# Kernel optimization log

Measured on AMD Instinct MI355X. Metric: run time of the kernel, lower is better.

The kernel has to match this reference:

```python
import jax, jax.numpy as jnp
import numpy as np

B, N, D_IN, D_OUT, E = 2, 50000, 128, 64, 800000
NEG_SLOPE = 0.2  # LeakyReLU negative slope (alpha)


def setup_inputs() -> dict:
    key = jax.random.key(0)
    ks = jax.random.split(key, 8)
    X_key = jax.random.normal(ks[0], (B, N, D_IN), dtype=jnp.float32)
    X_value = jax.random.normal(ks[1], (B, N, D_IN), dtype=jnp.float32)
    src = jax.random.randint(ks[2], (E,), 0, N, dtype=jnp.int32)
    dst = jnp.sort(jax.random.randint(ks[3], (E,), 0, N, dtype=jnp.int32))
    s = 1.0 / np.sqrt(D_IN)
    Wk = jax.random.normal(ks[4], (D_IN, D_OUT), dtype=jnp.float32) * s
    bk = jnp.zeros((D_OUT,), dtype=jnp.float32)
    Wv = jax.random.normal(ks[5], (D_IN, D_OUT), dtype=jnp.float32) * s
    bv = jnp.zeros((D_OUT,), dtype=jnp.float32)
    return {"X_key": X_key, "X_value": X_value, "Wk": Wk, "bk": bk,
            "Wv": Wv, "bv": bv, "src": src, "dst": dst}


def reference(X_key, X_value, Wk, bk, Wv, bv, src, dst):
    n = X_key.shape[1]
    h_key = X_key @ Wk + bk      # [B, N, D_OUT]
    h_value = X_value @ Wv + bv  # [B, N, D_OUT]

    def per_batch(hk, hv):
        # per-edge dot-product attention score
        e = jnp.sum(hk[src] * hk[dst], axis=-1)                    # [E]
        m = jax.lax.stop_gradient(jax.ops.segment_max(e, dst, num_segments=n))
        a = jnp.exp(e - m[dst])                                    # [E]
        denom = jax.ops.segment_sum(a, dst, num_segments=n)        # [N]
        num = jax.ops.segment_sum(a[:, None] * hv[src], dst, num_segments=n)  # [N, D_OUT]
        # nodes with no incoming edges get 0 (DGL leaves them zero-initialized)
        return num / jnp.where(denom == 0, 1.0, denom)[:, None]

    h_att = jax.vmap(per_batch)(h_key, h_value)  # [B, N, D_OUT]
    # LeakyReLU(alpha=0.2)
    return jnp.where(h_att >= 0, h_att, NEG_SLOPE * h_att)
```

## Files before the change

### kernel.cpp

```cpp
#include <hip/hip_runtime.h>
#include <cfloat>
#include <math.h>

#define D_IN 128
#define D_OUT 64
#define NEG_SLOPE 0.2f
#define ROWH 128
#define SQRT_LOG2E 1.2011224087864498f

typedef _Float16 half2v __attribute__((ext_vector_type(2)));
typedef _Float16 half8 __attribute__((ext_vector_type(8)));
typedef float f32x4 __attribute__((ext_vector_type(4)));

__device__ __forceinline__ unsigned short f2bf(float x) {
  union { float f; unsigned u; } a; a.f = x;
  unsigned r = a.u + 0x7FFFu + ((a.u >> 16) & 1u);
  return (unsigned short)(r >> 16);
}
__device__ __forceinline__ unsigned short f2h(float x) {
  union { _Float16 h; unsigned short u; } c;
  c.h = (_Float16)x;
  return c.u;
}
__device__ __forceinline__ float4 unpack_bf4(uint2 q) {
  union { unsigned u; float f; } t;
  float4 r;
  t.u = q.x << 16;          r.x = t.f;
  t.u = q.x & 0xFFFF0000u;  r.y = t.f;
  t.u = q.y << 16;          r.z = t.f;
  t.u = q.y & 0xFFFF0000u;  r.w = t.f;
  return r;
}
__device__ __forceinline__ float hdot4(uint2 a, uint2 b) {
  union { unsigned u; half2v h; } al, ah, bl, bh;
  al.u = a.x; ah.u = a.y; bl.u = b.x; bh.u = b.y;
#if __has_builtin(__builtin_amdgcn_fdot2)
  return __builtin_amdgcn_fdot2(al.h, bl.h,
         __builtin_amdgcn_fdot2(ah.h, bh.h, 0.f, false), false);
#else
  return (float)al.h[0] * (float)bl.h[0] + (float)al.h[1] * (float)bl.h[1] +
         (float)ah.h[0] * (float)bh.h[0] + (float)ah.h[1] * (float)bh.h[1];
#endif
}

__global__ void bfrag_kernel(const float* __restrict__ Wk,
                             const float* __restrict__ Wv,
                             _Float16* __restrict__ bfrag) {
  const int idx = blockIdx.x * 256 + threadIdx.x;
  if (idx >= 2048) return;
  const int which = idx >> 10;
  const float* __restrict__ W = which ? Wv : Wk;
  const float scale = which ? 1.0f : SQRT_LOG2E;
  const int li = idx & 1023;
  const int lane = li & 63;
  const int nt = (li >> 6) & 3;
  const int k0i = li >> 8;
  const int col = nt * 16 + (lane & 15);
  const int kbase = k0i * 32 + (lane >> 4) * 8;
  half8 h;
#pragma unroll
  for (int j = 0; j < 8; ++j)
    h[j] = (_Float16)(W[(size_t)(kbase + j) * D_OUT + col] * scale);
  reinterpret_cast<half8*>(bfrag)[idx] = h;
}

__global__ __launch_bounds__(256) void linear_mfma_kernel(
    const float* __restrict__ Xk, const float* __restrict__ Xv,
    const float* __restrict__ Wk, const float* __restrict__ bk,
    const float* __restrict__ Wv, const float* __restrict__ bv,
    const _Float16* __restrict__ bfrag, unsigned short* __restrict__ hkv,
    int R, int nblk) {
  const int which = (blockIdx.x >= nblk) ? 1 : 0;
  const int blk = blockIdx.x - which * nblk;
  const float* __restrict__ X = which ? Xv : Xk;
  const float* __restrict__ bias = which ? bv : bk;
  const float bscale = which ? 1.0f : SQRT_LOG2E;
  const int uoff = which ? D_OUT : 0;

  const int wave = threadIdx.x >> 6;
  const int lane = threadIdx.x & 63;
  const int r0 = (blk * 4 + wave) * 16;
  if (r0 >= R) return;
  const int rowi = lane & 15;
  const int kgrp = lane >> 4;

  if (r0 + 16 <= R) {
    const half8* btab =
        reinterpret_cast<const half8*>(bfrag) + (which ? 1024 : 0);
    half8 bf[4][4];
#pragma unroll
    for (int k0i = 0; k0i < 4; ++k0i)
#pragma unroll
      for (int nt = 0; nt < 4; ++nt)
        bf[k0i][nt] = btab[(k0i * 4 + nt) * 64 + lane];

    f32x4 acc[4];
#pragma unroll
    for (int nt = 0; nt < 4; ++nt) acc[nt] = (f32x4){0.f, 0.f, 0.f, 0.f};

    const float* xrow = X + (size_t)(r0 + rowi) * D_IN;
#pragma unroll
    for (int k0i = 0; k0i < 4; ++k0i) {
      const float4 x0 =
          *reinterpret_cast<const float4*>(xrow + k0i * 32 + kgrp * 8);
      const float4 x1 =
          *reinterpret_cast<const float4*>(xrow + k0i * 32 + kgrp * 8 + 4);
      half8 a;
      a[0] = (_Float16)x0.x; a[1] = (_Float16)x0.y;
      a[2] = (_Float16)x0.z; a[3] = (_Float16)x0.w;
      a[4] = (_Float16)x1.x; a[5] = (_Float16)x1.y;
      a[6] = (_Float16)x1.z; a[7] = (_Float16)x1.w;
#pragma unroll
      for (int nt = 0; nt < 4; ++nt)
        acc[nt] = __builtin_amdgcn_mfma_f32_16x16x32_f16(a, bf[k0i][nt],
                                                         acc[nt], 0, 0, 0);
    }
#pragma unroll
    for (int nt = 0; nt < 4; ++nt) {
      const int col = nt * 16 + rowi;
      const float bcol = bias[col] * bscale;
#pragma unroll
      for (int r = 0; r < 4; ++r) {
        const int row = r0 + kgrp * 4 + r;
        const float val = acc[nt][r] + bcol;
        hkv[(size_t)row * ROWH + uoff + col] =
            which ? f2bf(val) : f2h(val);
      }
    }
  } else {
    const float* __restrict__ W = which ? Wv : Wk;
    for (int r = r0; r < R; ++r) {
      const float* xr = X + (size_t)r * D_IN;
      float acc = bias[lane];
      for (int k = 0; k < D_IN; ++k)
        acc = fmaf(xr[k], W[(size_t)k * D_OUT + lane], acc);
      acc *= bscale;
      hkv[(size_t)r * ROWH + uoff + lane] = which ? f2bf(acc) : f2h(acc);
    }
  }
}

__global__ void rowptr_kernel(const int* __restrict__ dst, int E, int N,
                              int* __restrict__ row_ptr) {
  int i = blockIdx.x * blockDim.x + threadIdx.x;
  if (i > N) return;
  int lo = 0, hi = E;
  while (lo < hi) {
    int mid = (lo + hi) >> 1;
    if (dst[mid] < i) lo = mid + 1; else hi = mid;
  }
  row_ptr[i] = lo;
}

__device__ __forceinline__ float rowsum16(float p) {
  union { float f; int i; } u, v;
  u.f = p;
  v.i = __builtin_amdgcn_update_dpp(0, u.i, 0x121, 0xF, 0xF, true);
  u.f += v.f;
  v.i = __builtin_amdgcn_update_dpp(0, u.i, 0x122, 0xF, 0xF, true);
  u.f += v.f;
  v.i = __builtin_amdgcn_update_dpp(0, u.i, 0x124, 0xF, 0xF, true);
  u.f += v.f;
  v.i = __builtin_amdgcn_update_dpp(0, u.i, 0x128, 0xF, 0xF, true);
  u.f += v.f;
  return u.f;
}

struct SMState { float m, l; float4 a; };

__device__ __forceinline__ void sm_update(SMState& st, float pl,
                                          const uint2& vu) {
  if (pl > st.m) {
    const float sc = exp2f(st.m - pl);
    st.l *= sc;
    st.a.x *= sc; st.a.y *= sc; st.a.z *= sc; st.a.w *= sc;
    st.m = pl;
  }
  const float a = exp2f(pl - st.m);
  const float4 vs = unpack_bf4(vu);
  st.l += a;
  st.a.x = fmaf(a, vs.x, st.a.x);
  st.a.y = fmaf(a, vs.y, st.a.y);
  st.a.z = fmaf(a, vs.z, st.a.z);
  st.a.w = fmaf(a, vs.w, st.a.w);
}

__device__ __forceinline__ void sm_merge(SMState& d, const SMState& s) {
  const float mn = fmaxf(d.m, s.m);
  const float s1 = exp2f(d.m - mn);
  const float s2 = exp2f(s.m - mn);
  d.l = d.l * s1 + s.l * s2;
  d.a.x = d.a.x * s1 + s.a.x * s2;
  d.a.y = d.a.y * s1 + s.a.y * s2;
  d.a.z = d.a.z * s1 + s.a.z * s2;
  d.a.w = d.a.w * s1 + s.a.w * s2;
  d.m = mn;
}

__device__ __forceinline__ void sm_merge_xor(SMState& d, int off) {
  SMState s;
  s.m = __shfl_xor(d.m, off, 64);
  s.l = __shfl_xor(d.l, off, 64);
  s.a.x = __shfl_xor(d.a.x, off, 64);
  s.a.y = __shfl_xor(d.a.y, off, 64);
  s.a.z = __shfl_xor(d.a.z, off, 64);
  s.a.w = __shfl_xor(d.a.w, off, 64);
  sm_merge(d, s);
}

__global__ __launch_bounds__(256) void aggregate_kernel(
    const unsigned short* __restrict__ hkv, const int* __restrict__ src,
    const int* __restrict__ row_ptr, float* __restrict__ out, int N) {
  const int node = blockIdx.x * 4 + (threadIdx.x >> 6);
  const int lane = threadIdx.x & 63;
  if (node >= N) return;
  const unsigned short* hb0 = hkv;
  const unsigned short* hb1 = hkv + (size_t)N * ROWH;

  const int li = lane & 15;
  const int g = lane >> 4;

  const uint2 kd0 = reinterpret_cast<const uint2*>(hb0 + (size_t)node * ROWH)[li];
  const uint2 kd1 = reinterpret_cast<const uint2*>(hb1 + (size_t)node * ROWH)[li];
  const int e0 = row_ptr[node];
  const int e1 = row_ptr[node + 1];

  SMState A0 = {-FLT_MAX, 0.f, {0.f, 0.f, 0.f, 0.f}};
  SMState B0 = A0, A1 = A0, B1 = A0;

  int e = e0 + g;
  for (; e + 4 < e1; e += 8) {
    const int sA = src[e];
    const int sB = src[e + 4];
    const uint2* rA0 = reinterpret_cast<const uint2*>(hb0 + (size_t)sA * ROWH);
    const uint2* rA1 = reinterpret_cast<const uint2*>(hb1 + (size_t)sA * ROWH);
    const uint2* rB0 = reinterpret_cast<const uint2*>(hb0 + (size_t)sB * ROWH);
    const uint2* rB1 = reinterpret_cast<const uint2*>(hb1 + (size_t)sB * ROWH);
    const uint2 kA0 = rA0[li], vA0 = rA0[16 + li];
    const uint2 kA1 = rA1[li], vA1 = rA1[16 + li];
    const uint2 kB0 = rB0[li], vB0 = rB0[16 + li];
    const uint2 kB1 = rB1[li], vB1 = rB1[16 + li];

    const float plA0 = rowsum16(hdot4(kA0, kd0));
    const float plA1 = rowsum16(hdot4(kA1, kd1));
    const float plB0 = rowsum16(hdot4(kB0, kd0));
    const float plB1 = rowsum16(hdot4(kB1, kd1));

    sm_update(A0, plA0, vA0);
    sm_update(A1, plA1, vA1);
    sm_update(B0, plB0, vB0);
    sm_update(B1, plB1, vB1);
  }
  if (e < e1) {
    const int sA = src[e];
    const uint2* rA0 = reinterpret_cast<const uint2*>(hb0 + (size_t)sA * ROWH);
    const uint2* rA1 = reinterpret_cast<const uint2*>(hb1 + (size_t)sA * ROWH);
    const uint2 kA0 = rA0[li], vA0 = rA0[16 + li];
    const uint2 kA1 = rA1[li], vA1 = rA1[16 + li];
    const float plA0 = rowsum16(hdot4(kA0, kd0));
    const float plA1 = rowsum16(hdot4(kA1, kd1));
    sm_update(A0, plA0, vA0);
    sm_update(A1, plA1, vA1);
  }

  sm_merge(A0, B0);
  sm_merge(A1, B1);
  sm_merge_xor(A0, 16); sm_merge_xor(A0, 32);
  sm_merge_xor(A1, 16); sm_merge_xor(A1, 32);

  if (lane < 16) {
#pragma unroll
    for (int b = 0; b < 2; ++b) {
      const SMState& S = b ? A1 : A0;
      const float denom = (S.l == 0.f) ? 1.f : S.l;
      float4 o;
      o.x = S.a.x / denom; o.y = S.a.y / denom;
      o.z = S.a.z / denom; o.w = S.a.w / denom;
      o.x = (o.x >= 0.f) ? o.x : NEG_SLOPE * o.x;
      o.y = (o.y >= 0.f) ? o.y : NEG_SLOPE * o.y;
      o.z = (o.z >= 0.f) ? o.z : NEG_SLOPE * o.z;
      o.w = (o.w >= 0.f) ? o.w : NEG_SLOPE * o.w;
      *reinterpret_cast<float4*>(out + ((size_t)b * N + node) * D_OUT + 4 * lane) = o;
    }
  }
}

extern "C" void kernel_launch(void* const* d_in, const int* in_sizes, int n_in,
                              void* d_out, int out_size, void* d_ws,
                              size_t ws_size, hipStream_t stream) {
  const float* X_key   = (const float*)d_in[0];
  const float* X_value = (const float*)d_in[1];
  const float* Wk      = (const float*)d_in[2];
  const float* bk      = (const float*)d_in[3];
  const float* Wv      = (const float*)d_in[4];
  const float* bv      = (const float*)d_in[5];
  const int*   src     = (const int*)d_in[6];
  const int*   dst     = (const int*)d_in[7];
  float* out = (float*)d_out;

  const int B = 2;
  const int R = in_sizes[0] / D_IN;
  const int N = R / B;
  const int E = in_sizes[6];

  _Float16* bfrag = (_Float16*)d_ws;
  unsigned short* hkv = (unsigned short*)((char*)d_ws + 32768);
  int* row_ptr = (int*)(hkv + (size_t)R * ROWH);

  const int blocksB = (N + 1 + 255) / 256;
  hipLaunchKernelGGL(rowptr_kernel, dim3(blocksB), dim3(256), 0, stream,
                     dst, E, N, row_ptr);
  hipLaunchKernelGGL(bfrag_kernel, dim3(8), dim3(256), 0, stream,
                     Wk, Wv, bfrag);
  const int wavesPerMat = (R + 15) / 16;
  const int nblk = (wavesPerMat + 3) / 4;
  hipLaunchKernelGGL(linear_mfma_kernel, dim3(2 * nblk), dim3(256), 0, stream,
                     X_key, X_value, Wk, bk, Wv, bv, bfrag, hkv, R, nblk);
  const int blocksC = (N + 3) / 4;
  hipLaunchKernelGGL(aggregate_kernel, dim3(blocksC), dim3(256), 0, stream,
                     hkv, src, row_ptr, out, N);
}
```

Baseline: 100.2 us.

## Split aggregation per batch across blocks with XCD-aware block mapping

The aggregate kernel now gives each block a single batch instead of having every wave process both batches. Block IDs are mapped in groups of 8 so that each XCD-sized group handles one batch, aiming to keep each XCD's L2 working set to one batch's feature table. Each wave now keeps four independent edge streams per lane group instead of two per batch, preserving memory-level parallelism. The grid doubles in size, and the src indices and row_ptr are read twice, once per batch.

```diff
diff --git a/kernel.cpp b/kernel.cpp
--- a/kernel.cpp
+++ b/kernel.cpp
@@ -208,80 +208,69 @@
   sm_merge(d, s);
 }
 
+__device__ __forceinline__ void edge_proc(const unsigned short* __restrict__ hb,
+                                          int s, int li, const uint2& kd,
+                                          SMState& st) {
+  const uint2* r = reinterpret_cast<const uint2*>(hb + (size_t)s * ROWH);
+  const uint2 kq = r[li];
+  const uint2 vq = r[16 + li];
+  const float pl = rowsum16(hdot4(kq, kd));
+  sm_update(st, pl, vq);
+}
+
 __global__ __launch_bounds__(256) void aggregate_kernel(
     const unsigned short* __restrict__ hkv, const int* __restrict__ src,
-    const int* __restrict__ row_ptr, float* __restrict__ out, int N) {
-  const int node = blockIdx.x * 4 + (threadIdx.x >> 6);
+    const int* __restrict__ row_ptr, float* __restrict__ out, int N,
+    int nb4) {
+  const int b8 = blockIdx.x & 7;
+  const int batch = b8 >> 2;
+  const int idx = (blockIdx.x >> 3) * 4 + (b8 & 3);
+  if (idx >= nb4) return;
+  const int node = idx * 4 + (threadIdx.x >> 6);
   const int lane = threadIdx.x & 63;
   if (node >= N) return;
-  const unsigned short* hb0 = hkv;
-  const unsigned short* hb1 = hkv + (size_t)N * ROWH;
-
+
+  const unsigned short* hb = hkv + (size_t)batch * N * ROWH;
   const int li = lane & 15;
   const int g = lane >> 4;
 
-  const uint2 kd0 = reinterpret_cast<const uint2*>(hb0 + (size_t)node * ROWH)[li];
-  const uint2 kd1 = reinterpret_cast<const uint2*>(hb1 + (size_t)node * ROWH)[li];
+  const uint2 kd = reinterpret_cast<const uint2*>(hb + (size_t)node * ROWH)[li];
   const int e0 = row_ptr[node];
   const int e1 = row_ptr[node + 1];
 
-  SMState A0 = {-FLT_MAX, 0.f, {0.f, 0.f, 0.f, 0.f}};
-  SMState B0 = A0, A1 = A0, B1 = A0;
+  SMState A = {-FLT_MAX, 0.f, {0.f, 0.f, 0.f, 0.f}};
+  SMState B = A, C = A, D = A;
 
   int e = e0 + g;
-  for (; e + 4 < e1; e += 8) {
+  for (; e + 12 < e1; e += 16) {
     const int sA = src[e];
     const int sB = src[e + 4];
-    const uint2* rA0 = reinterpret_cast<const uint2*>(hb0 + (size_t)sA * ROWH);
-    const uint2* rA1 = reinterpret_cast<const uint2*>(hb1 + (size_t)sA * ROWH);
-    const uint2* rB0 = reinterpret_cast<const uint2*>(hb0 + (size_t)sB * ROWH);
-    const uint2* rB1 = reinterpret_cast<const uint2*>(hb1 + (size_t)sB * ROWH);
-    const uint2 kA0 = rA0[li], vA0 = rA0[16 + li];
-    const uint2 kA1 = rA1[li], vA1 = rA1[16 + li];
-    const uint2 kB0 = rB0[li], vB0 = rB0[16 + li];
-    const uint2 kB1 = rB1[li], vB1 = rB1[16 + li];
-
-    const float plA0 = rowsum16(hdot4(kA0, kd0));
-    const float plA1 = rowsum16(hdot4(kA1, kd1));
-    const float plB0 = rowsum16(hdot4(kB0, kd0));
-    const float plB1 = rowsum16(hdot4(kB1, kd1));
-
-    sm_update(A0, plA0, vA0);
-    sm_update(A1, plA1, vA1);
-    sm_update(B0, plB0, vB0);
-    sm_update(B1, plB1, vB1);
-  }
-  if (e < e1) {
-    const int sA = src[e];
-    const uint2* rA0 = reinterpret_cast<const uint2*>(hb0 + (size_t)sA * ROWH);
-    const uint2* rA1 = reinterpret_cast<const uint2*>(hb1 + (size_t)sA * ROWH);
-    const uint2 kA0 = rA0[li], vA0 = rA0[16 + li];
-    const uint2 kA1 = rA1[li], vA1 = rA1[16 + li];
-    const float plA0 = rowsum16(hdot4(kA0, kd0));
-    const float plA1 = rowsum16(hdot4(kA1, kd1));
-    sm_update(A0, plA0, vA0);
-    sm_update(A1, plA1, vA1);
-  }
-
-  sm_merge(A0, B0);
-  sm_merge(A1, B1);
-  sm_merge_xor(A0, 16); sm_merge_xor(A0, 32);
-  sm_merge_xor(A1, 16); sm_merge_xor(A1, 32);
+    const int sC = src[e + 8];
+    const int sD = src[e + 12];
+    edge_proc(hb, sA, li, kd, A);
+    edge_proc(hb, sB, li, kd, B);
+    edge_proc(hb, sC, li, kd, C);
+    edge_proc(hb, sD, li, kd, D);
+  }
+  for (; e < e1; e += 4) edge_proc(hb, src[e], li, kd, A);
+
+  sm_merge(A, B);
+  sm_merge(C, D);
+  sm_merge(A, C);
+  sm_merge_xor(A, 16);
+  sm_merge_xor(A, 32);
 
   if (lane < 16) {
-#pragma unroll
-    for (int b = 0; b < 2; ++b) {
-      const SMState& S = b ? A1 : A0;
-      const float denom = (S.l == 0.f) ? 1.f : S.l;
-      float4 o;
-      o.x = S.a.x / denom; o.y = S.a.y / denom;
-      o.z = S.a.z / denom; o.w = S.a.w / denom;
-      o.x = (o.x >= 0.f) ? o.x : NEG_SLOPE * o.x;
-      o.y = (o.y >= 0.f) ? o.y : NEG_SLOPE * o.y;
-      o.z = (o.z >= 0.f) ? o.z : NEG_SLOPE * o.z;
-      o.w = (o.w >= 0.f) ? o.w : NEG_SLOPE * o.w;
-      *reinterpret_cast<float4*>(out + ((size_t)b * N + node) * D_OUT + 4 * lane) = o;
-    }
+    const float denom = (A.l == 0.f) ? 1.f : A.l;
+    float4 o;
+    o.x = A.a.x / denom; o.y = A.a.y / denom;
+    o.z = A.a.z / denom; o.w = A.a.w / denom;
+    o.x = (o.x >= 0.f) ? o.x : NEG_SLOPE * o.x;
+    o.y = (o.y >= 0.f) ? o.y : NEG_SLOPE * o.y;
+    o.z = (o.z >= 0.f) ? o.z : NEG_SLOPE * o.z;
+    o.w = (o.w >= 0.f) ? o.w : NEG_SLOPE * o.w;
+    *reinterpret_cast<float4*>(out + ((size_t)batch * N + node) * D_OUT +
+                               4 * lane) = o;
   }
 }
 
@@ -316,7 +305,8 @@
   const int nblk = (wavesPerMat + 3) / 4;
   hipLaunchKernelGGL(linear_mfma_kernel, dim3(2 * nblk), dim3(256), 0, stream,
                      X_key, X_value, Wk, bk, Wv, bv, bfrag, hkv, R, nblk);
-  const int blocksC = (N + 3) / 4;
+  const int nb4 = (N + 3) / 4;
+  const int blocksC = ((2 * nb4 + 7) / 8) * 8;
   hipLaunchKernelGGL(aggregate_kernel, dim3(blocksC), dim3(256), 0, stream,
-                     hkv, src, row_ptr, out, N);
-}
+                     hkv, src, row_ptr, out, N, nb4);
+}
```

Measured after the change: 122.2 us. 1.22x slower.
